# Optimization experiments

Measured on AMD Instinct MI355X. Metric: run time of the kernel, lower is better.

The kernel has to match this reference:

```python
import jax, jax.numpy as jnp
import numpy as np

N_NODES, N_EDGES, N_GRAPHS = 100000, 1600000, 1000
DIN, DMID, DGLOB, DOUT = 128, 128, 64, 2


def setup_inputs() -> dict:
    key = jax.random.key(0)
    ks = jax.random.split(key, 12)
    x = jax.random.normal(ks[0], (N_NODES, DIN), dtype=jnp.float32)
    edge_index = jax.random.randint(ks[1], (2, N_EDGES), 0, N_NODES, dtype=jnp.int64 if jax.config.jax_enable_x64 else jnp.int32)
    u = jax.random.normal(ks[2], (N_GRAPHS, DGLOB), dtype=jnp.float32)
    batch = jnp.sort(jax.random.randint(ks[3], (N_NODES,), 0, N_GRAPHS))
    s = 1.0 / np.sqrt(DMID)
    W1 = jax.random.normal(ks[4], (DIN, DMID), dtype=jnp.float32) * s
    b1 = jnp.zeros((DMID,), dtype=jnp.float32)
    W2 = jax.random.normal(ks[5], (DMID, DMID), dtype=jnp.float32) * s
    b2 = jnp.zeros((DMID,), dtype=jnp.float32)
    Wh1 = jax.random.normal(ks[6], (DMID + DGLOB, DMID), dtype=jnp.float32) * s
    bh1 = jnp.zeros((DMID,), dtype=jnp.float32)
    Wh2 = jax.random.normal(ks[7], (DMID, DOUT), dtype=jnp.float32) * s
    bh2 = jnp.zeros((DOUT,), dtype=jnp.float32)
    return {"x": x, "edge_index": edge_index, "u": u, "batch": batch,
            "batch_size": N_GRAPHS, "W1": W1, "b1": b1, "W2": W2, "b2": b2,
            "Wh1": Wh1, "bh1": bh1, "Wh2": Wh2, "bh2": bh2}


def _gcn_conv(x, W, b, row, col, norm, n):
    # PyG GCNConv: linear transform then symmetric-normalized scatter-add
    h = x @ W                                    # [N, dmid]
    msg = norm[:, None] * h[row]                 # gather along source nodes
    out = jax.ops.segment_sum(msg, col, num_segments=n)  # scatter to dst
    return out + b


def reference(x, edge_index, u, batch, batch_size, W1, b1, W2, b2, Wh1, bh1, Wh2, bh2):
    n = x.shape[0]
    # add self-loops (GCNConv default, edge_weight=None -> all-ones weights)
    loop = jnp.arange(n, dtype=edge_index.dtype)
    row = jnp.concatenate([edge_index[0], loop])
    col = jnp.concatenate([edge_index[1], loop])
    deg = jax.ops.segment_sum(jnp.ones_like(col, dtype=x.dtype), col, num_segments=n)
    dinv = jnp.where(deg > 0, jax.lax.rsqrt(jnp.maximum(deg, 1e-12)), 0.0)
    norm = dinv[row] * dinv[col]                 # D^-1/2 A D^-1/2, shared by both layers

    h = jax.nn.relu(_gcn_conv(x, W1, b1, row, col, norm, n))
    h = jax.nn.relu(_gcn_conv(h, W2, b2, row, col, norm, n))

    # mean pool per graph
    sums = jax.ops.segment_sum(h, batch, num_segments=batch_size)
    cnt = jax.ops.segment_sum(jnp.ones((n,), dtype=h.dtype), batch, num_segments=batch_size)
    graph_emb = sums / jnp.maximum(cnt, 1.0)[:, None]

    hcat = jnp.concatenate([graph_emb, u], axis=-1)
    # head MLP (dropout in eval mode = identity)
    out = jax.nn.relu(hcat @ Wh1 + bh1) @ Wh2 + bh2
    return out
```

## Files before the change

kernel.cpp:

```cpp
#include <hip/hip_runtime.h>
#include <hip/hip_bf16.h>

#define NN 100000
#define NE 1600000
#define NG 1000
#define NBK 196
#define BSH 9
#define SLOT 10240

typedef short short8 __attribute__((ext_vector_type(8)));
typedef float f32x4 __attribute__((ext_vector_type(4)));
typedef float f32x2 __attribute__((ext_vector_type(2)));

static inline int cdiv(int a, int b) { return (a + b - 1) / b; }

__device__ __forceinline__ unsigned short f2b(float f) {
    unsigned int u = __float_as_uint(f);
    u += 0x7fff + ((u >> 16) & 1);
    return (unsigned short)(u >> 16);
}
__device__ __forceinline__ unsigned int pack2(float lo, float hi) {
    return (unsigned int)f2b(lo) | ((unsigned int)f2b(hi) << 16);
}

template <int W>
__device__ __forceinline__ f32x2 f8_2f(unsigned int v) {
    return __builtin_amdgcn_cvt_pk_f32_fp8((int)v, W);
}
__device__ __forceinline__ unsigned int f2f8_lo(float a, float b, unsigned int old) {
    return (unsigned int)__builtin_amdgcn_cvt_pk_fp8_f32(a, b, (int)old, false);
}
__device__ __forceinline__ unsigned int f2f8_hi(float a, float b, unsigned int old) {
    return (unsigned int)__builtin_amdgcn_cvt_pk_fp8_f32(a, b, (int)old, true);
}
__device__ __forceinline__ unsigned char f2f8s(float a) {
    return (unsigned char)(__builtin_amdgcn_cvt_pk_fp8_f32(a, a, 0, false) & 0xFF);
}

__global__ __launch_bounds__(256) void k_prep(const float* __restrict__ W1,
                                              const float* __restrict__ W2,
                                              const float* __restrict__ b1,
                                              const float* __restrict__ b2,
                                              unsigned short* __restrict__ Wt1,
                                              unsigned char* __restrict__ Wt2p,
                                              float* __restrict__ b1p,
                                              float* __restrict__ b2p,
                                              int* __restrict__ gcur,
                                              const int* __restrict__ batch,
                                              int* __restrict__ gstart) {
    int b = blockIdx.x, t = threadIdx.x;
    if (b < 128) {
        if (t < 128) {
            Wt1[b * 128 + t] = f2b(W1[t * 128 + b]);
        } else {
            int q = t - 128;
            int c = (q & 7) * 16 + (q >> 3);
            Wt2p[b * 128 + q] = f2f8s(W2[c * 128 + b]);
        }
    } else if (b == 128) {
        if (t < NBK) gcur[t] = t * SLOT;
        if (t < 128) {
            int c = (t & 7) * 16 + (t >> 3);
            b1p[t] = b1[c];
            b2p[t] = b2[c];
        }
    } else {
        int n = (b - 129) * 256 + t;
        if (n <= NN) {
            int cur = (n == NN) ? NG : batch[n];
            int prev = (n == 0) ? -1 : batch[n - 1];
            for (int g = prev + 1; g <= cur; g++) gstart[g] = n;
        }
    }
}

__global__ __launch_bounds__(256) void k_bin2(const int* __restrict__ row,
                                              const int* __restrict__ col,
                                              int* __restrict__ gcur,
                                              unsigned int* __restrict__ tmp) {
    __shared__ unsigned int ent[4000];
    __shared__ unsigned int srt[4000];
    __shared__ unsigned char bkt[4000];
    __shared__ unsigned char bky[4000];
    __shared__ int cnt[NBK];
    __shared__ int gbase[NBK];
    __shared__ int lbase[NBK];
    __shared__ int sh[256];
    int t = threadIdx.x;
    if (t < NBK) cnt[t] = 0;
    __syncthreads();
    const int q0 = blockIdx.x * 1000;
    const int4* col4 = (const int4*)col;
    const int4* row4 = (const int4*)row;
#pragma unroll
    for (int it = 0; it < 4; it++) {
        int idx = it * 256 + t;
        if (idx < 1000) {
            int4 c = col4[q0 + idx];
            int4 r = row4[q0 + idx];
            int d, b;
            d = c.x; b = d >> BSH; atomicAdd(&cnt[b], 1);
            ent[idx * 4 + 0] = ((unsigned int)(d & 511) << 17) | (unsigned int)r.x;
            bkt[idx * 4 + 0] = (unsigned char)b;
            d = c.y; b = d >> BSH; atomicAdd(&cnt[b], 1);
            ent[idx * 4 + 1] = ((unsigned int)(d & 511) << 17) | (unsigned int)r.y;
            bkt[idx * 4 + 1] = (unsigned char)b;
            d = c.z; b = d >> BSH; atomicAdd(&cnt[b], 1);
            ent[idx * 4 + 2] = ((unsigned int)(d & 511) << 17) | (unsigned int)r.z;
            bkt[idx * 4 + 2] = (unsigned char)b;
            d = c.w; b = d >> BSH; atomicAdd(&cnt[b], 1);
            ent[idx * 4 + 3] = ((unsigned int)(d & 511) << 17) | (unsigned int)r.w;
            bkt[idx * 4 + 3] = (unsigned char)b;
        }
    }
    __syncthreads();
    int v = (t < NBK) ? cnt[t] : 0;
    sh[t] = v;
    __syncthreads();
    for (int d = 1; d < 256; d <<= 1) {
        int u = (t >= d) ? sh[t - d] : 0;
        __syncthreads();
        sh[t] += u;
        __syncthreads();
    }
    if (t < NBK) {
        lbase[t] = sh[t] - v;
        gbase[t] = atomicAdd(&gcur[t], v);
        cnt[t] = sh[t] - v;
    }
    __syncthreads();
#pragma unroll
    for (int it = 0; it < 16; it++) {
        int i = it * 256 + t;
        if (i < 4000) {
            int b = bkt[i];
            int p = atomicAdd(&cnt[b], 1);
            srt[p] = ent[i];
            bky[p] = (unsigned char)b;
        }
    }
    __syncthreads();
#pragma unroll
    for (int it = 0; it < 16; it++) {
        int i = it * 256 + t;
        if (i < 4000) {
            int b = bky[i];
            tmp[gbase[b] + (i - lbase[b])] = srt[i];
        }
    }
}

__global__ __launch_bounds__(1024) void k_bucket(const unsigned int* __restrict__ tmp,
                                                 const int* __restrict__ gcur,
                                                 int* __restrict__ off,
                                                 int* __restrict__ degw,
                                                 float* __restrict__ dinv,
                                                 int* __restrict__ csr_src) {
    __shared__ int cnt[512];
    __shared__ int loff[512];
    __shared__ int sh[256];
    int b = blockIdx.x, t = threadIdx.x;
    int j0 = b << BSH;
    int nd = min(512, NN - j0);
    int rb = b * SLOT;
    int m = gcur[b] - rb;
    if (t < 512) cnt[t] = 0;
    __syncthreads();
    for (int i = t; i < m; i += 1024)
        atomicAdd(&cnt[tmp[rb + i] >> 17], 1);
    __syncthreads();
    int r0 = 0, r1 = 0, p0 = 0, ts = 0;
    if (t < 256) {
        r0 = cnt[2 * t]; r1 = cnt[2 * t + 1];
        p0 = (r0 + 3) & ~3;
        int p1 = (r1 + 3) & ~3;
        ts = p0 + p1;
        sh[t] = ts;
    }
    __syncthreads();
    for (int d = 1; d < 256; d <<= 1) {
        int u = (t >= d && t < 256) ? sh[t - d] : 0;
        __syncthreads();
        if (t < 256) sh[t] += u;
        __syncthreads();
    }
    if (t < 256) {
        int ex = sh[t] - ts;
        loff[2 * t] = ex;
        loff[2 * t + 1] = ex + p0;
    }
    __syncthreads();
    for (int j = t; j < nd; j += 1024) {
        int o = rb + loff[j];
        int dg = cnt[j];
        off[j0 + j] = o;
        degw[j0 + j] = dg;
        dinv[j0 + j] = rsqrtf((float)(dg + 1));
        cnt[j] = o;
    }
    __syncthreads();
    for (int i = t; i < m; i += 1024) {
        unsigned int e = tmp[rb + i];
        int d = e >> 17;
        int s = (int)(e & 0x1FFFFu);
        int p = atomicAdd(&cnt[d], 1);
        csr_src[p] = s;
    }
}

__global__ __launch_bounds__(256) void k_gemm1(const float* __restrict__ X,
                                               const unsigned short* __restrict__ Wt,
                                               const float* __restrict__ dinv,
                                               unsigned char* __restrict__ Hs8) {
    __shared__ __align__(16) unsigned short Ws[128 * 128];
    int t = threadIdx.x;
#pragma unroll
    for (int i = 0; i < 8; i++) {
        int id = t + i * 256;
        int n = id >> 4, c = id & 15;
        *(short8*)((char*)Ws + n * 256 + ((c ^ (n & 15)) << 4)) =
            *(const short8*)(Wt + n * 128 + c * 8);
    }
    __syncthreads();

    int lane = t & 63, wid = t >> 6;
    int n16 = lane & 15, quad = lane >> 4;
    int row_base = blockIdx.x * 128 + wid * 32;

    short8 a[2][4];
#pragma unroll
    for (int rt = 0; rt < 2; rt++) {
        int r = row_base + rt * 16 + n16;
        if (r > NN - 1) r = NN - 1;
        const float* ap = X + (size_t)r * 128 + quad * 8;
#pragma unroll
        for (int ks = 0; ks < 4; ks++) {
            float4 v0 = *(const float4*)(ap + ks * 32);
            float4 v1 = *(const float4*)(ap + ks * 32 + 4);
            uint4 up;
            up.x = pack2(v0.x, v0.y); up.y = pack2(v0.z, v0.w);
            up.z = pack2(v1.x, v1.y); up.w = pack2(v1.z, v1.w);
            a[rt][ks] = *(short8*)&up;
        }
    }

    f32x4 acc[2][8];
#pragma unroll
    for (int rt = 0; rt < 2; rt++)
#pragma unroll
        for (int ct = 0; ct < 8; ct++)
            acc[rt][ct] = (f32x4){0.f, 0.f, 0.f, 0.f};

#pragma unroll
    for (int ks = 0; ks < 4; ks++) {
#pragma unroll
        for (int ct = 0; ct < 8; ct++) {
            short8 b = *(const short8*)((const char*)Ws +
                        (ct * 16 + n16) * 256 + ((((ks << 2) + quad) ^ n16) << 4));
            acc[0][ct] = __builtin_amdgcn_mfma_f32_16x16x32_bf16(a[0][ks], b, acc[0][ct], 0, 0, 0);
            acc[1][ct] = __builtin_amdgcn_mfma_f32_16x16x32_bf16(a[1][ks], b, acc[1][ct], 0, 0, 0);
        }
    }

#pragma unroll
    for (int rt = 0; rt < 2; rt++) {
#pragma unroll
        for (int reg = 0; reg < 4; reg++) {
            int row = row_base + rt * 16 + quad * 4 + reg;
            if (row < NN) {
                float di = dinv[row];
                unsigned int u0 = 0, u1 = 0;
                u0 = f2f8_lo(acc[rt][0][reg] * di, acc[rt][1][reg] * di, u0);
                u0 = f2f8_hi(acc[rt][2][reg] * di, acc[rt][3][reg] * di, u0);
                u1 = f2f8_lo(acc[rt][4][reg] * di, acc[rt][5][reg] * di, u1);
                u1 = f2f8_hi(acc[rt][6][reg] * di, acc[rt][7][reg] * di, u1);
                uint2 o; o.x = u0; o.y = u1;
                ((uint2*)(Hs8 + (size_t)row * 128))[n16] = o;
            }
        }
    }
}

__global__ __launch_bounds__(256) void k_gemm2(const unsigned char* __restrict__ A8,
                                               const unsigned char* __restrict__ Wt2p,
                                               const float* __restrict__ dinv,
                                               unsigned char* __restrict__ Hs8) {
    __shared__ __align__(16) unsigned char Ws[128 * 128];
    int t = threadIdx.x;
#pragma unroll
    for (int i = 0; i < 8; i++) {
        int id = t + i * 256;
        int n = id >> 4, c = id & 15;
        *(uint2*)(Ws + n * 128 + ((c ^ (n & 15)) << 3)) =
            *(const uint2*)(Wt2p + n * 128 + c * 8);
    }
    __syncthreads();

    int lane = t & 63, wid = t >> 6;
    int n16 = lane & 15, quad = lane >> 4;
    int row_base = blockIdx.x * 128 + wid * 32;

    uint2 a[2][4];
#pragma unroll
    for (int rt = 0; rt < 2; rt++) {
        int r = row_base + rt * 16 + n16;
        if (r > NN - 1) r = NN - 1;
        const unsigned char* ap = A8 + (size_t)r * 128 + quad * 8;
#pragma unroll
        for (int ks = 0; ks < 4; ks++)
            a[rt][ks] = *(const uint2*)(ap + ks * 32);
    }

    f32x4 acc[2][8];
#pragma unroll
    for (int rt = 0; rt < 2; rt++)
#pragma unroll
        for (int ct = 0; ct < 8; ct++)
            acc[rt][ct] = (f32x4){0.f, 0.f, 0.f, 0.f};

#pragma unroll
    for (int ks = 0; ks < 4; ks++) {
        long a0 = __builtin_bit_cast(long, a[0][ks]);
        long a1 = __builtin_bit_cast(long, a[1][ks]);
#pragma unroll
        for (int ct = 0; ct < 8; ct++) {
            uint2 bv = *(const uint2*)(Ws + (ct * 16 + n16) * 128 +
                                       ((((ks << 2) + quad) ^ n16) << 3));
            long bb = __builtin_bit_cast(long, bv);
            acc[0][ct] = __builtin_amdgcn_mfma_f32_16x16x32_fp8_fp8(a0, bb, acc[0][ct], 0, 0, 0);
            acc[1][ct] = __builtin_amdgcn_mfma_f32_16x16x32_fp8_fp8(a1, bb, acc[1][ct], 0, 0, 0);
        }
    }

#pragma unroll
    for (int rt = 0; rt < 2; rt++) {
#pragma unroll
        for (int reg = 0; reg < 4; reg++) {
            int row = row_base + rt * 16 + quad * 4 + reg;
            if (row < NN) {
                float di = dinv[row];
                unsigned int u0 = 0, u1 = 0;
                u0 = f2f8_lo(acc[rt][0][reg] * di, acc[rt][1][reg] * di, u0);
                u0 = f2f8_hi(acc[rt][2][reg] * di, acc[rt][3][reg] * di, u0);
                u1 = f2f8_lo(acc[rt][4][reg] * di, acc[rt][5][reg] * di, u1);
                u1 = f2f8_hi(acc[rt][6][reg] * di, acc[rt][7][reg] * di, u1);
                uint2 o; o.x = u0; o.y = u1;
                ((uint2*)(Hs8 + (size_t)row * 128))[n16] = o;
            }
        }
    }
}

__global__ __launch_bounds__(256) void k_agg(const unsigned char* __restrict__ Hb,
                                             const int* __restrict__ off,
                                             const int* __restrict__ degw,
                                             const int* __restrict__ csr_src,
                                             const float* __restrict__ dinv,
                                             const float* __restrict__ biasp,
                                             unsigned char* __restrict__ outp) {
    int node = blockIdx.x * 16 + (threadIdx.x >> 4);
    int li = threadIdx.x & 15;
    unsigned loff = (unsigned)li * 8u;
    f32x2 A0 = {0.f, 0.f}, A1 = {0.f, 0.f}, A2 = {0.f, 0.f}, A3 = {0.f, 0.f};
#define LDH(idx) (*(const uint2*)(Hb + (unsigned)(idx) * 128u + loff))
#define ACC8(V) { \
        A0 += f8_2f<0>((V).x); A1 += f8_2f<1>((V).x); \
        A2 += f8_2f<0>((V).y); A3 += f8_2f<1>((V).y); }
    int deg = degw[node];
    int base = off[node];
    uint2 v = LDH(node);
    ACC8(v)
    for (int e = 0; e < deg; e += 4) {
        int4 ix = *(const int4*)(csr_src + base + e);
        uint2 w0 = LDH(ix.x);
        uint2 w1 = {0, 0}, w2 = {0, 0}, w3 = {0, 0};
        if (e + 1 < deg) w1 = LDH(ix.y);
        if (e + 2 < deg) w2 = LDH(ix.z);
        if (e + 3 < deg) w3 = LDH(ix.w);
        ACC8(w0) ACC8(w1) ACC8(w2) ACC8(w3)
    }
#undef ACC8
#undef LDH
    float di = dinv[node];
    const float4* b4 = (const float4*)biasp;
    float4 bA = b4[li * 2], bB = b4[li * 2 + 1];
    float r0 = fmaxf(fmaf(di, A0[0], bA.x), 0.f);
    float r1 = fmaxf(fmaf(di, A0[1], bA.y), 0.f);
    float r2 = fmaxf(fmaf(di, A1[0], bA.z), 0.f);
    float r3 = fmaxf(fmaf(di, A1[1], bA.w), 0.f);
    float r4 = fmaxf(fmaf(di, A2[0], bB.x), 0.f);
    float r5 = fmaxf(fmaf(di, A2[1], bB.y), 0.f);
    float r6 = fmaxf(fmaf(di, A3[0], bB.z), 0.f);
    float r7 = fmaxf(fmaf(di, A3[1], bB.w), 0.f);
    unsigned int u0 = 0, u1 = 0;
    u0 = f2f8_lo(r0, r1, u0); u0 = f2f8_hi(r2, r3, u0);
    u1 = f2f8_lo(r4, r5, u1); u1 = f2f8_hi(r6, r7, u1);
    uint2 o; o.x = u0; o.y = u1;
    *(uint2*)(outp + (unsigned)node * 128u + loff) = o;
}

__global__ __launch_bounds__(256) void k_poolhead(const unsigned char* __restrict__ A,
                                                  const int* __restrict__ gstart,
                                                  const float* __restrict__ u,
                                                  const float* __restrict__ Wh1,
                                                  const float* __restrict__ bh1,
                                                  const float* __restrict__ Wh2,
                                                  const float* __restrict__ bh2,
                                                  float* __restrict__ out) {
    int g = blockIdx.x, t = threadIdx.x;
    int start = gstart[g];
    int end = gstart[g + 1];

    int li = t & 7;
    int ri = t >> 3;
    float acc[16];
#pragma unroll
    for (int j = 0; j < 16; j++) acc[j] = 0.f;
    f32x2 p;
    for (int i = start + ri; i < end; i += 32) {
        uint4 v = ((const uint4*)A)[(size_t)i * 8 + li];
#define UP(VV, base) p = f8_2f<0>(VV); acc[base] += p.x; acc[base+1] += p.y; \
                     p = f8_2f<1>(VV); acc[base+2] += p.x; acc[base+3] += p.y;
        UP(v.x, 0) UP(v.y, 4) UP(v.z, 8) UP(v.w, 12)
#undef UP
    }
#pragma unroll
    for (int j = 0; j < 16; j++) {
        acc[j] += __shfl_xor(acc[j], 8);
        acc[j] += __shfl_xor(acc[j], 16);
        acc[j] += __shfl_xor(acc[j], 32);
    }
    __shared__ float part[4][128];
    __shared__ float hc[192];
    __shared__ float tt[128];
    int w = t >> 6;
    if ((t & 63) < 8) {
#pragma unroll
        for (int j = 0; j < 16; j++) part[w][li * 16 + j] = acc[j];
    }
    __syncthreads();
    float cntf = (float)max(end - start, 1);
    if (t < 128) {
        int q = (t & 15) * 8 + (t >> 4);
        hc[t] = (part[0][q] + part[1][q] + part[2][q] + part[3][q]) / cntf;
    } else if (t < 192) {
        hc[t] = u[g * 64 + (t - 128)];
    }
    __syncthreads();
    if (t < 128) {
        float a2 = bh1[t];
        for (int k = 0; k < 192; k++) a2 = fmaf(hc[k], Wh1[k * 128 + t], a2);
        tt[t] = fmaxf(a2, 0.f);
    }
    __syncthreads();
    if (t < 2) {
        float o = bh2[t];
        for (int c2 = 0; c2 < 128; c2++) o = fmaf(tt[c2], Wh2[c2 * 2 + t], o);
        out[g * 2 + t] = o;
    }
}

extern "C" void kernel_launch(void* const* d_in, const int* in_sizes, int n_in,
                              void* d_out, int out_size, void* d_ws, size_t ws_size,
                              hipStream_t stream) {
    const float* x   = (const float*)d_in[0];
    const int*   ei  = (const int*)d_in[1];
    const int*   row = ei;
    const int*   col = ei + NE;
    const float* u   = (const float*)d_in[2];
    const int*   batch = (const int*)d_in[3];
    const float* W1  = (const float*)d_in[5];
    const float* b1  = (const float*)d_in[6];
    const float* W2  = (const float*)d_in[7];
    const float* b2  = (const float*)d_in[8];
    const float* Wh1 = (const float*)d_in[9];
    const float* bh1 = (const float*)d_in[10];
    const float* Wh2 = (const float*)d_in[11];
    const float* bh2 = (const float*)d_in[12];
    float* out = (float*)d_out;

    char* ws = (char*)d_ws;
    size_t o = 0;
    auto alloc = [&](size_t bytes) -> void* {
        void* p = ws + o;
        o += (bytes + 511) & ~(size_t)511;
        return p;
    };
    unsigned char*  Hs8 = (unsigned char*)alloc((size_t)NN * 128);
    unsigned char*  A1b = (unsigned char*)alloc((size_t)NN * 128);
    unsigned char*  A2b = (unsigned char*)alloc((size_t)NN * 128);
    unsigned short* Wt1 = (unsigned short*)alloc((size_t)128 * 128 * 2);
    unsigned char*  Wt2p= (unsigned char*)alloc((size_t)128 * 128);
    float* b1p    = (float*)alloc((size_t)128 * 4);
    float* b2p    = (float*)alloc((size_t)128 * 4);
    float* dinv   = (float*)alloc((size_t)NN * 4);
    int*   off    = (int*)alloc((size_t)NN * 4);
    int*   degw   = (int*)alloc((size_t)NN * 4);
    int*   csr_src= (int*)alloc((size_t)NBK * SLOT * 4 + 256);
    unsigned int* tmp = (unsigned int*)alloc((size_t)NBK * SLOT * 4);
    int*   gcur   = (int*)alloc((size_t)256 * 4);
    int*   gstart = (int*)alloc((size_t)(NG + 1) * 4);

    k_prep<<<129 + cdiv(NN + 1, 256), 256, 0, stream>>>(W1, W2, b1, b2, Wt1, Wt2p,
                                                        b1p, b2p, gcur, batch, gstart);
    k_bin2<<<400, 256, 0, stream>>>(row, col, gcur, tmp);
    k_bucket<<<NBK, 1024, 0, stream>>>(tmp, gcur, off, degw, dinv, csr_src);

    k_gemm1<<<cdiv(NN, 128), 256, 0, stream>>>(x, Wt1, dinv, Hs8);
    k_agg<<<NN / 16, 256, 0, stream>>>(Hs8, off, degw, csr_src, dinv, b1p, A1b);
    k_gemm2<<<cdiv(NN, 128), 256, 0, stream>>>(A1b, Wt2p, dinv, Hs8);
    k_agg<<<NN / 16, 256, 0, stream>>>(Hs8, off, degw, csr_src, dinv, b2p, A2b);

    k_poolhead<<<NG, 256, 0, stream>>>(A2b, gstart, u, Wh1, bh1, Wh2, bh2, out);
}
```

Measured before the change: 259.3 us.

## Pad CSR rows to multiples of eight with dummy zero node and unroll aggregation

Pads each destination's CSR adjacency list to a multiple of 8 entries, filling the padding with a sentinel index that points at a zero row appended to the fp8 feature buffer, so the aggregation loop needs no per-edge bounds checks. Offset and padded degree are packed into one meta word, replacing two separate arrays. The aggregation kernel now processes 16 neighbours per iteration and prefetches the next batch of indices to keep more gathers in flight. In exchange, CSR storage grows, k_bucket spends extra time writing padding, and padded slots add wasted gathers of the zero row.

```diff
diff --git a/kernel.cpp b/kernel.cpp
--- a/kernel.cpp
+++ b/kernel.cpp
@@ -7,6 +7,7 @@
 #define NBK 196
 #define BSH 9
 #define SLOT 10240
+#define SLOTC 12288
 
 typedef short short8 __attribute__((ext_vector_type(8)));
 typedef float f32x4 __attribute__((ext_vector_type(4)));
@@ -47,7 +48,8 @@
                                               float* __restrict__ b2p,
                                               int* __restrict__ gcur,
                                               const int* __restrict__ batch,
-                                              int* __restrict__ gstart) {
+                                              int* __restrict__ gstart,
+                                              unsigned char* __restrict__ Hs8) {
     int b = blockIdx.x, t = threadIdx.x;
     if (b < 128) {
         if (t < 128) {
@@ -63,6 +65,10 @@
             int c = (t & 7) * 16 + (t >> 3);
             b1p[t] = b1[c];
             b2p[t] = b2[c];
+        }
+        if (t >= 128 && t < 136) {
+            uint4 z; z.x = 0u; z.y = 0u; z.z = 0u; z.w = 0u;
+            ((uint4*)(Hs8 + (size_t)NN * 128))[t - 128] = z;
         }
     } else {
         int n = (b - 129) * 256 + t;
@@ -152,17 +158,18 @@
 
 __global__ __launch_bounds__(1024) void k_bucket(const unsigned int* __restrict__ tmp,
                                                  const int* __restrict__ gcur,
-                                                 int* __restrict__ off,
-                                                 int* __restrict__ degw,
+                                                 unsigned int* __restrict__ meta,
                                                  float* __restrict__ dinv,
                                                  int* __restrict__ csr_src) {
     __shared__ int cnt[512];
     __shared__ int loff[512];
+    __shared__ int send[512];
     __shared__ int sh[256];
     int b = blockIdx.x, t = threadIdx.x;
     int j0 = b << BSH;
     int nd = min(512, NN - j0);
     int rb = b * SLOT;
+    int rbc = b * SLOTC;
     int m = gcur[b] - rb;
     if (t < 512) cnt[t] = 0;
     __syncthreads();
@@ -172,8 +179,8 @@
     int r0 = 0, r1 = 0, p0 = 0, ts = 0;
     if (t < 256) {
         r0 = cnt[2 * t]; r1 = cnt[2 * t + 1];
-        p0 = (r0 + 3) & ~3;
-        int p1 = (r1 + 3) & ~3;
+        p0 = (r0 + 7) & ~7;
+        int p1 = (r1 + 7) & ~7;
         ts = p0 + p1;
         sh[t] = ts;
     }
@@ -191,10 +198,11 @@
     }
     __syncthreads();
     for (int j = t; j < nd; j += 1024) {
-        int o = rb + loff[j];
+        int o = rbc + loff[j];
         int dg = cnt[j];
-        off[j0 + j] = o;
-        degw[j0 + j] = dg;
+        int dgp = (dg + 7) & ~7;
+        meta[j0 + j] = (unsigned int)o | ((unsigned int)dgp << 22);
+        send[j] = o + dgp;
         dinv[j0 + j] = rsqrtf((float)(dg + 1));
         cnt[j] = o;
     }
@@ -205,6 +213,11 @@
         int s = (int)(e & 0x1FFFFu);
         int p = atomicAdd(&cnt[d], 1);
         csr_src[p] = s;
+    }
+    __syncthreads();
+    for (int j = t; j < nd; j += 1024) {
+        int pe = send[j];
+        for (int p = cnt[j]; p < pe; p++) csr_src[p] = NN;
     }
 }
 
@@ -352,32 +365,43 @@
 }
 
 __global__ __launch_bounds__(256) void k_agg(const unsigned char* __restrict__ Hb,
-                                             const int* __restrict__ off,
-                                             const int* __restrict__ degw,
+                                             const unsigned int* __restrict__ meta,
                                              const int* __restrict__ csr_src,
                                              const float* __restrict__ dinv,
                                              const float* __restrict__ biasp,
                                              unsigned char* __restrict__ outp) {
     int node = blockIdx.x * 16 + (threadIdx.x >> 4);
     int li = threadIdx.x & 15;
-    unsigned loff = (unsigned)li * 8u;
+    unsigned lo8 = (unsigned)li * 8u;
+    unsigned int md = meta[node];
+    int base = (int)(md & 0x3FFFFFu);
+    int degp = (int)(md >> 22);
     f32x2 A0 = {0.f, 0.f}, A1 = {0.f, 0.f}, A2 = {0.f, 0.f}, A3 = {0.f, 0.f};
-#define LDH(idx) (*(const uint2*)(Hb + (unsigned)(idx) * 128u + loff))
+#define LDH(idx) (*(const uint2*)(Hb + (unsigned)(idx) * 128u + lo8))
 #define ACC8(V) { \
         A0 += f8_2f<0>((V).x); A1 += f8_2f<1>((V).x); \
         A2 += f8_2f<0>((V).y); A3 += f8_2f<1>((V).y); }
-    int deg = degw[node];
-    int base = off[node];
     uint2 v = LDH(node);
+    const int4* ip = (const int4*)(csr_src + base);
+    int4 i0 = ip[0], i1 = ip[1], i2 = ip[2], i3 = ip[3];
     ACC8(v)
-    for (int e = 0; e < deg; e += 4) {
-        int4 ix = *(const int4*)(csr_src + base + e);
-        uint2 w0 = LDH(ix.x);
-        uint2 w1 = {0, 0}, w2 = {0, 0}, w3 = {0, 0};
-        if (e + 1 < deg) w1 = LDH(ix.y);
-        if (e + 2 < deg) w2 = LDH(ix.z);
-        if (e + 3 < deg) w3 = LDH(ix.w);
+    for (int e0 = 0; e0 < degp; e0 += 16) {
+        uint2 w0 = LDH(i0.x), w1 = LDH(i0.y), w2 = LDH(i0.z), w3 = LDH(i0.w);
+        uint2 w4 = LDH(i1.x), w5 = LDH(i1.y), w6 = LDH(i1.z), w7 = LDH(i1.w);
+        uint2 w8 = {0, 0}, w9 = {0, 0}, wA = {0, 0}, wB = {0, 0};
+        uint2 wC = {0, 0}, wD = {0, 0}, wE = {0, 0}, wF = {0, 0};
+        if (e0 + 8 < degp) {
+            w8 = LDH(i2.x); w9 = LDH(i2.y); wA = LDH(i2.z); wB = LDH(i2.w);
+            wC = LDH(i3.x); wD = LDH(i3.y); wE = LDH(i3.z); wF = LDH(i3.w);
+        }
+        if (e0 + 16 < degp) {
+            const int4* np = (const int4*)(csr_src + base + e0 + 16);
+            i0 = np[0]; i1 = np[1]; i2 = np[2]; i3 = np[3];
+        }
         ACC8(w0) ACC8(w1) ACC8(w2) ACC8(w3)
+        ACC8(w4) ACC8(w5) ACC8(w6) ACC8(w7)
+        ACC8(w8) ACC8(w9) ACC8(wA) ACC8(wB)
+        ACC8(wC) ACC8(wD) ACC8(wE) ACC8(wF)
     }
 #undef ACC8
 #undef LDH
@@ -396,7 +420,7 @@
     u0 = f2f8_lo(r0, r1, u0); u0 = f2f8_hi(r2, r3, u0);
     u1 = f2f8_lo(r4, r5, u1); u1 = f2f8_hi(r6, r7, u1);
     uint2 o; o.x = u0; o.y = u1;
-    *(uint2*)(outp + (unsigned)node * 128u + loff) = o;
+    *(uint2*)(outp + (unsigned)node * 128u + lo8) = o;
 }
 
 __global__ __launch_bounds__(256) void k_poolhead(const unsigned char* __restrict__ A,
@@ -486,7 +510,7 @@
         o += (bytes + 511) & ~(size_t)511;
         return p;
     };
-    unsigned char*  Hs8 = (unsigned char*)alloc((size_t)NN * 128);
+    unsigned char*  Hs8 = (unsigned char*)alloc((size_t)(NN + 1) * 128);
     unsigned char*  A1b = (unsigned char*)alloc((size_t)NN * 128);
     unsigned char*  A2b = (unsigned char*)alloc((size_t)NN * 128);
     unsigned short* Wt1 = (unsigned short*)alloc((size_t)128 * 128 * 2);
@@ -494,22 +518,21 @@
     float* b1p    = (float*)alloc((size_t)128 * 4);
     float* b2p    = (float*)alloc((size_t)128 * 4);
     float* dinv   = (float*)alloc((size_t)NN * 4);
-    int*   off    = (int*)alloc((size_t)NN * 4);
-    int*   degw   = (int*)alloc((size_t)NN * 4);
-    int*   csr_src= (int*)alloc((size_t)NBK * SLOT * 4 + 256);
+    unsigned int* meta = (unsigned int*)alloc((size_t)NN * 4);
+    int*   csr_src= (int*)alloc((size_t)NBK * SLOTC * 4 + 512);
     unsigned int* tmp = (unsigned int*)alloc((size_t)NBK * SLOT * 4);
     int*   gcur   = (int*)alloc((size_t)256 * 4);
     int*   gstart = (int*)alloc((size_t)(NG + 1) * 4);
 
     k_prep<<<129 + cdiv(NN + 1, 256), 256, 0, stream>>>(W1, W2, b1, b2, Wt1, Wt2p,
-                                                        b1p, b2p, gcur, batch, gstart);
+                                                        b1p, b2p, gcur, batch, gstart, Hs8);
     k_bin2<<<400, 256, 0, stream>>>(row, col, gcur, tmp);
-    k_bucket<<<NBK, 1024, 0, stream>>>(tmp, gcur, off, degw, dinv, csr_src);
+    k_bucket<<<NBK, 1024, 0, stream>>>(tmp, gcur, meta, dinv, csr_src);
 
     k_gemm1<<<cdiv(NN, 128), 256, 0, stream>>>(x, Wt1, dinv, Hs8);
-    k_agg<<<NN / 16, 256, 0, stream>>>(Hs8, off, degw, csr_src, dinv, b1p, A1b);
+    k_agg<<<NN / 16, 256, 0, stream>>>(Hs8, meta, csr_src, dinv, b1p, A1b);
     k_gemm2<<<cdiv(NN, 128), 256, 0, stream>>>(A1b, Wt2p, dinv, Hs8);
-    k_agg<<<NN / 16, 256, 0, stream>>>(Hs8, off, degw, csr_src, dinv, b2p, A2b);
+    k_agg<<<NN / 16, 256, 0, stream>>>(Hs8, meta, csr_src, dinv, b2p, A2b);
 
     k_poolhead<<<NG, 256, 0, stream>>>(A2b, gstart, u, Wh1, bh1, Wh2, bh2, out);
 }
```

Result: faster. 238.7 us (-8.0%).
